# Kernel optimization log

Hardware: AMD Instinct MI355X
Metric: run time of the kernel (lower is better)

The kernel has to match this reference:

```python
import jax, jax.numpy as jnp
import numpy as np

N = 100000   # nodes
E = 1600000  # edges
DIN, DH, DOUT = 64, 128, 128


def setup_inputs() -> dict:
    key = jax.random.key(0)
    ks = jax.random.split(key, 12)
    x = jax.random.normal(ks[0], (N, DIN), dtype=jnp.float32)
    edge_index = jax.random.randint(ks[1], (2, E), 0, N, dtype=jnp.int32)
    s = 1.0 / np.sqrt(DIN)
    W1 = jax.random.uniform(ks[2], (DIN, DH), jnp.float32, -s, s)
    b1 = jnp.zeros((DH,), jnp.float32)
    g1 = jnp.ones((DH,), jnp.float32)
    bt1 = jnp.zeros((DH,), jnp.float32)
    s2 = 1.0 / np.sqrt(DH)
    W2 = jax.random.uniform(ks[3], (DH, DOUT), jnp.float32, -s2, s2)
    b2 = jnp.zeros((DOUT,), jnp.float32)
    g2 = jnp.ones((DOUT,), jnp.float32)
    bt2 = jnp.zeros((DOUT,), jnp.float32)
    return {"x": x, "edge_index": edge_index, "W1": W1, "b1": b1, "g1": g1,
            "bt1": bt1, "W2": W2, "b2": b2, "g2": g2, "bt2": bt2}


def _layer_norm(h, g, b, eps=1e-5):
    mu = h.mean(-1, keepdims=True)
    var = h.var(-1, keepdims=True)
    return (h - mu) * jax.lax.rsqrt(var + eps) * g + b


def reference(x, edge_index, W1, b1, g1, bt1, W2, b2, g2, bt2):
    # GCN normalization with self-loops (shared graph structure for both layers)
    src, dst = edge_index[0], edge_index[1]
    loops = jnp.arange(N, dtype=src.dtype)
    src = jnp.concatenate([src, loops])
    dst = jnp.concatenate([dst, loops])
    deg = jax.ops.segment_sum(jnp.ones_like(src, jnp.float32), dst, num_segments=N)
    dinv = jnp.where(deg > 0, jax.lax.rsqrt(deg), 0.0)
    norm = dinv[src] * dinv[dst]  # [E+N]

    def gcn(h, W, b):
        hw = h @ W                         # linear first (PyG GCNConv)
        msg = hw[src] * norm[:, None]      # gather + edge scale
        return jax.ops.segment_sum(msg, dst, num_segments=N) + b

    h = jax.nn.relu(_layer_norm(gcn(x, W1, b1), g1, bt1))
    # dropout is identity at inference
    h = jax.nn.relu(_layer_norm(gcn(h, W2, b2), g2, bt2))
    return h
```

## Files before the change

### kernel.cpp

```cpp
#include <hip/hip_runtime.h>

#define NN 100000
#define NE 1600000
#define NBKT 196
#define CAP 12288
#define EPB 2048
#define ABLK ((NE + EPB - 1) / EPB)
typedef unsigned short u16;
typedef unsigned int u32;

typedef __attribute__((ext_vector_type(8))) short short8v;
typedef __attribute__((ext_vector_type(4))) float f32x4;

__device__ __forceinline__ u32 f2bf(float f) {
    u32 u = __float_as_uint(f);
    return (u + 0x7fffu + ((u >> 16) & 1u)) >> 16;
}
__device__ __forceinline__ u32 pack2(float a, float b) {
    return f2bf(a) | (f2bf(b) << 16);
}
__device__ __forceinline__ void accum8(float* a, uint4 u, float w) {
    a[0] += __uint_as_float(u.x << 16) * w;
    a[1] += __uint_as_float(u.x & 0xffff0000u) * w;
    a[2] += __uint_as_float(u.y << 16) * w;
    a[3] += __uint_as_float(u.y & 0xffff0000u) * w;
    a[4] += __uint_as_float(u.z << 16) * w;
    a[5] += __uint_as_float(u.z & 0xffff0000u) * w;
    a[6] += __uint_as_float(u.w << 16) * w;
    a[7] += __uint_as_float(u.w & 0xffff0000u) * w;
}

__global__ __launch_bounds__(256) void kA_bin(const int* __restrict__ src,
                                              const int* __restrict__ dst,
                                              int* __restrict__ gcnt,
                                              u32* __restrict__ binned) {
    __shared__ int bc[NBKT];
    __shared__ int cbase[NBKT];
    const int tid = threadIdx.x;
    for (int i = tid; i < NBKT; i += 256) bc[i] = 0;
    __syncthreads();
    const int e0 = blockIdx.x * EPB;
#pragma unroll
    for (int i = 0; i < EPB / 256; ++i) {
        const int e = e0 + i * 256 + tid;
        if (e < NE) atomicAdd(&bc[dst[e] >> 9], 1);
    }
    __syncthreads();
    for (int i = tid; i < NBKT; i += 256)
        cbase[i] = bc[i] ? atomicAdd(&gcnt[i], bc[i]) : 0;
    __syncthreads();
    for (int i = tid; i < NBKT; i += 256) bc[i] = 0;
    __syncthreads();
#pragma unroll
    for (int i = 0; i < EPB / 256; ++i) {
        const int e = e0 + i * 256 + tid;
        if (e < NE) {
            const int d = dst[e];
            const int bkt = d >> 9;
            const int p = atomicAdd(&bc[bkt], 1);
            binned[bkt * CAP + cbase[bkt] + p] = ((u32)src[e] << 9) | (u32)(d & 511);
        }
    }
}

__global__ __launch_bounds__(256) void kB_fill(const u32* __restrict__ binned,
                                               const int* __restrict__ gcnt,
                                               int2* __restrict__ off2,
                                               float* __restrict__ dinv,
                                               int* __restrict__ csr,
                                               const float* __restrict__ x,
                                               u16* __restrict__ xb) {
    __shared__ int lcnt[512];
    __shared__ int lpos[512];
    __shared__ float sdinv[512];
    __shared__ int ws[4];
    const int b = blockIdx.x;
    const int tid = threadIdx.x;
    const int cnt = gcnt[b];
    const int base0 = b * CAP;
    const int node0 = b << 9;
    lcnt[tid] = 0;
    lcnt[tid + 256] = 0;
    __syncthreads();
    for (int e = tid; e < cnt; e += 256)
        atomicAdd(&lcnt[binned[base0 + e] & 511], 1);
    __syncthreads();
    const int c0 = lcnt[tid * 2], c1 = lcnt[tid * 2 + 1];
    const int s = c0 + c1;
    const int lane = tid & 63, w = tid >> 6;
    int incl = s;
#pragma unroll
    for (int o = 1; o < 64; o <<= 1) {
        const int u = __shfl_up(incl, o);
        if (lane >= o) incl += u;
    }
    if (lane == 63) ws[w] = incl;
    __syncthreads();
    int base = incl - s;
    for (int i = 0; i < w; ++i) base += ws[i];
    lpos[tid * 2] = base;
    lpos[tid * 2 + 1] = base + c0;
    const float d0 = rsqrtf(1.0f + (float)c0);
    const float d1 = rsqrtf(1.0f + (float)c1);
    sdinv[tid * 2] = d0;
    sdinv[tid * 2 + 1] = d1;
    const int n0 = node0 + tid * 2;
    if (n0 < NN) {
        off2[n0] = make_int2(base0 + base, base0 + base + c0);
        dinv[n0] = d0;
    }
    if (n0 + 1 < NN) {
        off2[n0 + 1] = make_int2(base0 + base + c0, base0 + base + c0 + c1);
        dinv[n0 + 1] = d1;
    }
    __syncthreads();
    for (int e = tid; e < cnt; e += 256) {
        const u32 u = binned[base0 + e];
        const int p = atomicAdd(&lpos[u & 511], 1);
        csr[base0 + p] = (int)(u >> 9);
    }
    const int nmax = min(512, NN - node0);
    for (int gi = tid; gi < nmax * 8; gi += 256) {
        const int nl = gi >> 3, ch = gi & 7;
        const float dr = sdinv[nl];
        const size_t xo = (size_t)(node0 + nl) * 64 + ch * 8;
        const float4 v0 = *(const float4*)&x[xo];
        const float4 v1 = *(const float4*)&x[xo + 4];
        uint4 o;
        o.x = pack2(v0.x * dr, v0.y * dr); o.y = pack2(v0.z * dr, v0.w * dr);
        o.z = pack2(v1.x * dr, v1.y * dr); o.w = pack2(v1.z * dr, v1.w * dr);
        *(uint4*)&xb[xo] = o;
    }
}

__global__ __launch_bounds__(256) void k_prep(const float* __restrict__ W1,
                                              const float* __restrict__ W2,
                                              u16* __restrict__ WT1,
                                              u16* __restrict__ WT2,
                                              int* __restrict__ gcnt) {
    const int i = blockIdx.x * 256 + threadIdx.x;
    if (i < 8192) {
        const int k = i >> 7, c = i & 127;
        WT1[c * 64 + k] = (u16)f2bf(W1[i]);
    } else if (i < 24576) {
        const int i2 = i - 8192;
        const int k = i2 >> 7, c = i2 & 127;
        WT2[c * 128 + k] = (u16)f2bf(W2[i2]);
    } else if (i < 24576 + NBKT) {
        gcnt[i - 24576] = 0;
    }
}

template<int K, bool FP32OUT, bool PRESCALE>
__global__ __launch_bounds__(256) void k_fused(const u16* __restrict__ A,
                                               const int2* __restrict__ off2,
                                               const int* __restrict__ csr,
                                               const float* __restrict__ dinv,
                                               const u16* __restrict__ WT,
                                               const float* __restrict__ bias,
                                               const float* __restrict__ g,
                                               const float* __restrict__ bt,
                                               void* __restrict__ outp) {
    constexpr int RB = K * 2;
    constexpr int SUBS = 512 / K;
    constexpr int LSH = (K == 64) ? 7 : 8;
    __shared__ u16 As[4 * 16 * K];
    const int tid = threadIdx.x;
    const int wv = tid >> 6, lane = tid & 63;
    const int sub = lane / (64 / SUBS);
    const int l = lane & (64 / SUBS - 1);
    const char* Ab = (const char*)A + ((u32)l << 4);
    char* myAs = (char*)As + wv * 16 * RB;
    const int nodeBase = blockIdx.x * 64 + wv * 16;

    for (int i = 0; i < 16; ++i) {
        const int node = min(nodeBase + i, NN - 1);
        const float di = dinv[node];
        float a[8] = {};
        {
            const uint4 u = *(const uint4*)(Ab + ((u32)node << LSH));
            accum8(a, u, (sub == 0) ? 1.0f : 0.0f);
        }
        const int2 oe = off2[node];
        int base = oe.x;
        const int e1 = oe.y;
        u32 iA = 0, iB = 0, iC = 0;
        float vA = 0.f, vB = 0.f, vC = 0.f;
        if (base < e1) {
            const int eA = base + sub, eB = eA + SUBS, eC = eA + 2 * SUBS;
            iA = (u32)csr[min(eA, e1 - 1)];
            iB = (u32)csr[min(eB, e1 - 1)];
            iC = (u32)csr[min(eC, e1 - 1)];
            vA = (eA < e1) ? 1.f : 0.f;
            vB = (eB < e1) ? 1.f : 0.f;
            vC = (eC < e1) ? 1.f : 0.f;
        }
        while (base < e1) {
            const uint4 uA = *(const uint4*)(Ab + (iA << LSH));
            const uint4 uB = *(const uint4*)(Ab + (iB << LSH));
            const uint4 uC = *(const uint4*)(Ab + (iC << LSH));
            const float wA = vA, wB = vB, wC = vC;
            base += 3 * SUBS;
            if (base < e1) {
                const int eA = base + sub, eB = eA + SUBS, eC = eA + 2 * SUBS;
                iA = (u32)csr[min(eA, e1 - 1)];
                iB = (u32)csr[min(eB, e1 - 1)];
                iC = (u32)csr[min(eC, e1 - 1)];
                vA = (eA < e1) ? 1.f : 0.f;
                vB = (eB < e1) ? 1.f : 0.f;
                vC = (eC < e1) ? 1.f : 0.f;
            }
            accum8(a, uA, wA);
            accum8(a, uB, wB);
            accum8(a, uC, wC);
        }
#pragma unroll
        for (int t = 0; t < 8; ++t)
#pragma unroll
            for (int o = 64 / SUBS; o < 64; o <<= 1)
                a[t] += __shfl_xor(a[t], o);
        if (sub == 0) {
            uint4 o;
            o.x = pack2(a[0] * di, a[1] * di); o.y = pack2(a[2] * di, a[3] * di);
            o.z = pack2(a[4] * di, a[5] * di); o.w = pack2(a[6] * di, a[7] * di);
            *(uint4*)(myAs + i * RB + (((u32)l << 4) ^ ((u32)(i & 7) << 4))) = o;
        }
    }

    const int lr = lane & 15, kg = lane >> 4;
    short8v af[K / 32];
#pragma unroll
    for (int kk = 0; kk < K / 32; ++kk)
        af[kk] = *(const short8v*)(myAs + lr * RB +
                                   ((u32)(kk * 64 + kg * 16) ^ ((u32)(lr & 7) << 4)));
    f32x4 acc[8];
#pragma unroll
    for (int nt = 0; nt < 8; ++nt) {
        acc[nt] = (f32x4){0.f, 0.f, 0.f, 0.f};
        const int col = nt * 16 + lr;
        short8v bf[K / 32];
#pragma unroll
        for (int kk = 0; kk < K / 32; ++kk)
            bf[kk] = *(const short8v*)&WT[col * K + kk * 32 + kg * 8];
#pragma unroll
        for (int kk = 0; kk < K / 32; ++kk)
            acc[nt] = __builtin_amdgcn_mfma_f32_16x16x32_bf16(af[kk], bf[kk], acc[nt], 0, 0, 0);
    }

    float s1[4] = {0.f, 0.f, 0.f, 0.f};
    float s2[4] = {0.f, 0.f, 0.f, 0.f};
#pragma unroll
    for (int nt = 0; nt < 8; ++nt) {
        const float bvn = bias[nt * 16 + lr];
#pragma unroll
        for (int j = 0; j < 4; ++j) {
            const float v = acc[nt][j] + bvn;
            acc[nt][j] = v;
            s1[j] += v;
            s2[j] += v * v;
        }
    }
#pragma unroll
    for (int j = 0; j < 4; ++j)
#pragma unroll
        for (int o = 1; o < 16; o <<= 1) {
            s1[j] += __shfl_xor(s1[j], o);
            s2[j] += __shfl_xor(s2[j], o);
        }
    float mu4[4], rs4[4], dr4[4];
    int wr4[4];
#pragma unroll
    for (int j = 0; j < 4; ++j) {
        const int node = nodeBase + kg * 4 + j;
        wr4[j] = node < NN;
        const float mu = s1[j] * (1.0f / 128.0f);
        const float var = s2[j] * (1.0f / 128.0f) - mu * mu;
        mu4[j] = mu;
        rs4[j] = rsqrtf(var + 1e-5f);
        dr4[j] = PRESCALE ? dinv[min(node, NN - 1)] : 1.0f;
    }
#pragma unroll
    for (int nt = 0; nt < 8; ++nt) {
        const int col = nt * 16 + lr;
        const float gvn = g[col];
        const float tvn = bt[col];
#pragma unroll
        for (int j = 0; j < 4; ++j) {
            if (wr4[j]) {
                const int node = nodeBase + kg * 4 + j;
                const float y = fmaxf((acc[nt][j] - mu4[j]) * rs4[j] * gvn + tvn, 0.f) * dr4[j];
                if constexpr (FP32OUT)
                    ((float*)outp)[(size_t)node * 128 + col] = y;
                else
                    ((u16*)outp)[(size_t)node * 128 + col] = (u16)f2bf(y);
            }
        }
    }
}

extern "C" void kernel_launch(void* const* d_in, const int* in_sizes, int n_in,
                              void* d_out, int out_size, void* d_ws, size_t ws_size,
                              hipStream_t stream) {
    const float* x   = (const float*)d_in[0];
    const int*   ei  = (const int*)d_in[1];
    const float* W1  = (const float*)d_in[2];
    const float* b1  = (const float*)d_in[3];
    const float* g1  = (const float*)d_in[4];
    const float* bt1 = (const float*)d_in[5];
    const float* W2  = (const float*)d_in[6];
    const float* b2  = (const float*)d_in[7];
    const float* g2  = (const float*)d_in[8];
    const float* bt2 = (const float*)d_in[9];

    const int* src = ei;
    const int* dst = ei + NE;

    const int NP = (NN + 255) & ~255;
    int*   gcnt   = (int*)d_ws;
    int2*  off2   = (int2*)(gcnt + 256);
    float* dinv   = (float*)(off2 + NP);
    int*   csr    = (int*)(dinv + NP);
    u32*   binned = (u32*)(csr + NBKT * CAP);
    u16*   xb     = (u16*)(binned + NBKT * CAP);
    u16*   h1     = xb + (size_t)NN * 64;
    u16*   WT1    = h1 + (size_t)NN * 128;
    u16*   WT2    = WT1 + 128 * 64;

    k_prep<<<(24576 + NBKT + 255) / 256, 256, 0, stream>>>(W1, W2, WT1, WT2, gcnt);
    kA_bin<<<ABLK, 256, 0, stream>>>(src, dst, gcnt, binned);
    kB_fill<<<NBKT, 256, 0, stream>>>(binned, gcnt, off2, dinv, csr, x, xb);

    k_fused<64, false, true><<<(NN + 63) / 64, 256, 0, stream>>>(
        xb, off2, csr, dinv, WT1, b1, g1, bt1, h1);

    k_fused<128, true, false><<<(NN + 63) / 64, 256, 0, stream>>>(
        h1, off2, csr, dinv, WT2, b2, g2, bt2, d_out);
}
```

Baseline: 236.5 us.

## Balance gather across waves via LDS work claiming and split GEMM columns

Each block now handles 32 nodes instead of 64. Waves claim nodes dynamically through an LDS atomic counter, so uneven per-node degrees no longer leave some waves idle while others finish their fixed 16-node slice. The MFMA stage is repartitioned so each wave computes 32 output columns for all 32 rows. Because of this the LayerNorm statistics are reduced across waves through shared memory, which adds two block barriers and an LDS reduction. The bounds clamps are dropped, which relies on NN being divisible by 32.

```diff
diff --git a/kernel.cpp b/kernel.cpp
--- a/kernel.cpp
+++ b/kernel.cpp
@@ -164,17 +164,25 @@
     constexpr int RB = K * 2;
     constexpr int SUBS = 512 / K;
     constexpr int LSH = (K == 64) ? 7 : 8;
-    __shared__ u16 As[4 * 16 * K];
+    __shared__ u16 As[32 * K];
+    __shared__ float s1s[4][32];
+    __shared__ float s2s[4][32];
+    __shared__ int claim;
     const int tid = threadIdx.x;
     const int wv = tid >> 6, lane = tid & 63;
     const int sub = lane / (64 / SUBS);
     const int l = lane & (64 / SUBS - 1);
     const char* Ab = (const char*)A + ((u32)l << 4);
-    char* myAs = (char*)As + wv * 16 * RB;
-    const int nodeBase = blockIdx.x * 64 + wv * 16;
-
-    for (int i = 0; i < 16; ++i) {
-        const int node = min(nodeBase + i, NN - 1);
+    const int nodeBase = blockIdx.x * 32;
+
+    if (tid == 0) claim = 0;
+    __syncthreads();
+
+    int i;
+    if (lane == 0) i = atomicAdd(&claim, 1);
+    i = __builtin_amdgcn_readfirstlane(i);
+    while (i < 32) {
+        const int node = nodeBase + i;
         const float di = dinv[node];
         float a[8] = {};
         {
@@ -223,79 +231,96 @@
             uint4 o;
             o.x = pack2(a[0] * di, a[1] * di); o.y = pack2(a[2] * di, a[3] * di);
             o.z = pack2(a[4] * di, a[5] * di); o.w = pack2(a[6] * di, a[7] * di);
-            *(uint4*)(myAs + i * RB + (((u32)l << 4) ^ ((u32)(i & 7) << 4))) = o;
-        }
-    }
+            *(uint4*)((char*)As + i * RB + (((u32)l << 4) ^ ((u32)(i & 7) << 4))) = o;
+        }
+        if (lane == 0) i = atomicAdd(&claim, 1);
+        i = __builtin_amdgcn_readfirstlane(i);
+    }
+    __syncthreads();
 
     const int lr = lane & 15, kg = lane >> 4;
-    short8v af[K / 32];
-#pragma unroll
-    for (int kk = 0; kk < K / 32; ++kk)
-        af[kk] = *(const short8v*)(myAs + lr * RB +
-                                   ((u32)(kk * 64 + kg * 16) ^ ((u32)(lr & 7) << 4)));
-    f32x4 acc[8];
-#pragma unroll
-    for (int nt = 0; nt < 8; ++nt) {
-        acc[nt] = (f32x4){0.f, 0.f, 0.f, 0.f};
-        const int col = nt * 16 + lr;
+    short8v af[2][K / 32];
+#pragma unroll
+    for (int rt = 0; rt < 2; ++rt)
+#pragma unroll
+        for (int kk = 0; kk < K / 32; ++kk)
+            af[rt][kk] = *(const short8v*)((const char*)As + (rt * 16 + lr) * RB +
+                                           ((u32)(kk * 64 + kg * 16) ^ ((u32)(lr & 7) << 4)));
+    f32x4 acc[2][2];
+    float bv[2], gv[2], tv[2];
+#pragma unroll
+    for (int nt = 0; nt < 2; ++nt) {
+        acc[0][nt] = (f32x4){0.f, 0.f, 0.f, 0.f};
+        acc[1][nt] = (f32x4){0.f, 0.f, 0.f, 0.f};
+        const int col = wv * 32 + nt * 16 + lr;
         short8v bf[K / 32];
 #pragma unroll
         for (int kk = 0; kk < K / 32; ++kk)
             bf[kk] = *(const short8v*)&WT[col * K + kk * 32 + kg * 8];
 #pragma unroll
-        for (int kk = 0; kk < K / 32; ++kk)
-            acc[nt] = __builtin_amdgcn_mfma_f32_16x16x32_bf16(af[kk], bf[kk], acc[nt], 0, 0, 0);
-    }
-
-    float s1[4] = {0.f, 0.f, 0.f, 0.f};
-    float s2[4] = {0.f, 0.f, 0.f, 0.f};
-#pragma unroll
-    for (int nt = 0; nt < 8; ++nt) {
-        const float bvn = bias[nt * 16 + lr];
+        for (int rt = 0; rt < 2; ++rt)
+#pragma unroll
+            for (int kk = 0; kk < K / 32; ++kk)
+                acc[rt][nt] = __builtin_amdgcn_mfma_f32_16x16x32_bf16(
+                    af[rt][kk], bf[kk], acc[rt][nt], 0, 0, 0);
+        bv[nt] = bias[col]; gv[nt] = g[col]; tv[nt] = bt[col];
+    }
+
+    float s1[2][4] = {};
+    float s2[2][4] = {};
+#pragma unroll
+    for (int rt = 0; rt < 2; ++rt)
+#pragma unroll
+        for (int nt = 0; nt < 2; ++nt)
+#pragma unroll
+            for (int j = 0; j < 4; ++j) {
+                const float v = acc[rt][nt][j] + bv[nt];
+                acc[rt][nt][j] = v;
+                s1[rt][j] += v;
+                s2[rt][j] += v * v;
+            }
+#pragma unroll
+    for (int rt = 0; rt < 2; ++rt)
+#pragma unroll
+        for (int j = 0; j < 4; ++j)
+#pragma unroll
+            for (int o = 1; o < 16; o <<= 1) {
+                s1[rt][j] += __shfl_xor(s1[rt][j], o);
+                s2[rt][j] += __shfl_xor(s2[rt][j], o);
+            }
+    if (lr == 0) {
+#pragma unroll
+        for (int rt = 0; rt < 2; ++rt)
+#pragma unroll
+            for (int j = 0; j < 4; ++j) {
+                s1s[wv][rt * 16 + kg * 4 + j] = s1[rt][j];
+                s2s[wv][rt * 16 + kg * 4 + j] = s2[rt][j];
+            }
+    }
+    __syncthreads();
+
+#pragma unroll
+    for (int rt = 0; rt < 2; ++rt)
 #pragma unroll
         for (int j = 0; j < 4; ++j) {
-            const float v = acc[nt][j] + bvn;
-            acc[nt][j] = v;
-            s1[j] += v;
-            s2[j] += v * v;
-        }
-    }
-#pragma unroll
-    for (int j = 0; j < 4; ++j)
-#pragma unroll
-        for (int o = 1; o < 16; o <<= 1) {
-            s1[j] += __shfl_xor(s1[j], o);
-            s2[j] += __shfl_xor(s2[j], o);
-        }
-    float mu4[4], rs4[4], dr4[4];
-    int wr4[4];
-#pragma unroll
-    for (int j = 0; j < 4; ++j) {
-        const int node = nodeBase + kg * 4 + j;
-        wr4[j] = node < NN;
-        const float mu = s1[j] * (1.0f / 128.0f);
-        const float var = s2[j] * (1.0f / 128.0f) - mu * mu;
-        mu4[j] = mu;
-        rs4[j] = rsqrtf(var + 1e-5f);
-        dr4[j] = PRESCALE ? dinv[min(node, NN - 1)] : 1.0f;
-    }
-#pragma unroll
-    for (int nt = 0; nt < 8; ++nt) {
-        const int col = nt * 16 + lr;
-        const float gvn = g[col];
-        const float tvn = bt[col];
-#pragma unroll
-        for (int j = 0; j < 4; ++j) {
-            if (wr4[j]) {
-                const int node = nodeBase + kg * 4 + j;
-                const float y = fmaxf((acc[nt][j] - mu4[j]) * rs4[j] * gvn + tvn, 0.f) * dr4[j];
+            const int row = rt * 16 + kg * 4 + j;
+            const float t1 = s1s[0][row] + s1s[1][row] + s1s[2][row] + s1s[3][row];
+            const float t2 = s2s[0][row] + s2s[1][row] + s2s[2][row] + s2s[3][row];
+            const float mu = t1 * (1.0f / 128.0f);
+            const float var = t2 * (1.0f / 128.0f) - mu * mu;
+            const float rs = rsqrtf(var + 1e-5f);
+            const int node = nodeBase + row;
+            const float dr = PRESCALE ? dinv[node] : 1.0f;
+#pragma unroll
+            for (int nt = 0; nt < 2; ++nt) {
+                const float y = fmaxf((acc[rt][nt][j] - mu) * rs * gv[nt] + tv[nt], 0.f) * dr;
+                const int col = wv * 32 + nt * 16 + lr;
                 if constexpr (FP32OUT)
                     ((float*)outp)[(size_t)node * 128 + col] = y;
                 else
                     ((u16*)outp)[(size_t)node * 128 + col] = (u16)f2bf(y);
             }
         }
-    }
 }
 
 extern "C" void kernel_launch(void* const* d_in, const int* in_sizes, int n_in,
@@ -330,9 +355,9 @@
     kA_bin<<<ABLK, 256, 0, stream>>>(src, dst, gcnt, binned);
     kB_fill<<<NBKT, 256, 0, stream>>>(binned, gcnt, off2, dinv, csr, x, xb);
 
-    k_fused<64, false, true><<<(NN + 63) / 64, 256, 0, stream>>>(
+    k_fused<64, false, true><<<NN / 32, 256, 0, stream>>>(
         xb, off2, csr, dinv, WT1, b1, g1, bt1, h1);
 
-    k_fused<128, true, false><<<(NN + 63) / 64, 256, 0, stream>>>(
+    k_fused<128, true, false><<<NN / 32, 256, 0, stream>>>(
         h1, off2, csr, dinv, WT2, b2, g2, bt2, d_out);
 }
```

Result: faster. 201.2 us (-15.0%).

## Dynamically distribute block's 64 nodes across wavefronts via LDS atomic counter

Applied to the files above, without the earlier changes.

Replaces the static assignment of 16 nodes per wavefront with a shared-memory atomic work counter, so each of the 4 wavefronts claims the next node to aggregate until all 64 are done. The goal is to balance uneven per-node degree across wavefronts within a block and reduce idle time before the MFMA stage. In exchange it adds an LDS atomic and readfirstlane per node plus a block-wide barrier before the matmul, since rows can now be written by any wavefront.

```diff
diff --git a/kernel.cpp b/kernel.cpp
--- a/kernel.cpp
+++ b/kernel.cpp
@@ -164,43 +164,35 @@
     constexpr int RB = K * 2;
     constexpr int SUBS = 512 / K;
     constexpr int LSH = (K == 64) ? 7 : 8;
-    __shared__ u16 As[4 * 16 * K];
+    __shared__ u16 As[64 * K];
+    __shared__ int claim;
     const int tid = threadIdx.x;
     const int wv = tid >> 6, lane = tid & 63;
     const int sub = lane / (64 / SUBS);
     const int l = lane & (64 / SUBS - 1);
     const char* Ab = (const char*)A + ((u32)l << 4);
-    char* myAs = (char*)As + wv * 16 * RB;
-    const int nodeBase = blockIdx.x * 64 + wv * 16;
-
-    for (int i = 0; i < 16; ++i) {
-        const int node = min(nodeBase + i, NN - 1);
-        const float di = dinv[node];
-        float a[8] = {};
-        {
-            const uint4 u = *(const uint4*)(Ab + ((u32)node << LSH));
-            accum8(a, u, (sub == 0) ? 1.0f : 0.0f);
-        }
-        const int2 oe = off2[node];
-        int base = oe.x;
-        const int e1 = oe.y;
-        u32 iA = 0, iB = 0, iC = 0;
-        float vA = 0.f, vB = 0.f, vC = 0.f;
-        if (base < e1) {
-            const int eA = base + sub, eB = eA + SUBS, eC = eA + 2 * SUBS;
-            iA = (u32)csr[min(eA, e1 - 1)];
-            iB = (u32)csr[min(eB, e1 - 1)];
-            iC = (u32)csr[min(eC, e1 - 1)];
-            vA = (eA < e1) ? 1.f : 0.f;
-            vB = (eB < e1) ? 1.f : 0.f;
-            vC = (eC < e1) ? 1.f : 0.f;
-        }
-        while (base < e1) {
-            const uint4 uA = *(const uint4*)(Ab + (iA << LSH));
-            const uint4 uB = *(const uint4*)(Ab + (iB << LSH));
-            const uint4 uC = *(const uint4*)(Ab + (iC << LSH));
-            const float wA = vA, wB = vB, wC = vC;
-            base += 3 * SUBS;
+    const int nodeBase = blockIdx.x * 64;
+
+    if (tid == 0) claim = 0;
+    __syncthreads();
+
+    int i;
+    if (lane == 0) i = atomicAdd(&claim, 1);
+    i = __builtin_amdgcn_readfirstlane(i);
+    while (i < 64) {
+        const int node = nodeBase + i;
+        if (node < NN) {
+            const float di = dinv[node];
+            float a[8] = {};
+            {
+                const uint4 u = *(const uint4*)(Ab + ((u32)node << LSH));
+                accum8(a, u, (sub == 0) ? 1.0f : 0.0f);
+            }
+            const int2 oe = off2[node];
+            int base = oe.x;
+            const int e1 = oe.y;
+            u32 iA = 0, iB = 0, iC = 0;
+            float vA = 0.f, vB = 0.f, vC = 0.f;
             if (base < e1) {
                 const int eA = base + sub, eB = eA + SUBS, eC = eA + 2 * SUBS;
                 iA = (u32)csr[min(eA, e1 - 1)];
@@ -210,29 +202,54 @@
                 vB = (eB < e1) ? 1.f : 0.f;
                 vC = (eC < e1) ? 1.f : 0.f;
             }
-            accum8(a, uA, wA);
-            accum8(a, uB, wB);
-            accum8(a, uC, wC);
-        }
-#pragma unroll
-        for (int t = 0; t < 8; ++t)
-#pragma unroll
-            for (int o = 64 / SUBS; o < 64; o <<= 1)
-                a[t] += __shfl_xor(a[t], o);
-        if (sub == 0) {
-            uint4 o;
-            o.x = pack2(a[0] * di, a[1] * di); o.y = pack2(a[2] * di, a[3] * di);
-            o.z = pack2(a[4] * di, a[5] * di); o.w = pack2(a[6] * di, a[7] * di);
-            *(uint4*)(myAs + i * RB + (((u32)l << 4) ^ ((u32)(i & 7) << 4))) = o;
-        }
-    }
+            while (base < e1) {
+                const uint4 uA = *(const uint4*)(Ab + (iA << LSH));
+                const uint4 uB = *(const uint4*)(Ab + (iB << LSH));
+                const uint4 uC = *(const uint4*)(Ab + (iC << LSH));
+                const float wA = vA, wB = vB, wC = vC;
+                base += 3 * SUBS;
+                if (base < e1) {
+                    const int eA = base + sub, eB = eA + SUBS, eC = eA + 2 * SUBS;
+                    iA = (u32)csr[min(eA, e1 - 1)];
+                    iB = (u32)csr[min(eB, e1 - 1)];
+                    iC = (u32)csr[min(eC, e1 - 1)];
+                    vA = (eA < e1) ? 1.f : 0.f;
+                    vB = (eB < e1) ? 1.f : 0.f;
+                    vC = (eC < e1) ? 1.f : 0.f;
+                }
+                accum8(a, uA, wA);
+                accum8(a, uB, wB);
+                accum8(a, uC, wC);
+            }
+#pragma unroll
+            for (int t = 0; t < 8; ++t)
+#pragma unroll
+                for (int o = 64 / SUBS; o < 64; o <<= 1)
+                    a[t] += __shfl_xor(a[t], o);
+            if (sub == 0) {
+                uint4 o;
+                o.x = pack2(a[0] * di, a[1] * di); o.y = pack2(a[2] * di, a[3] * di);
+                o.z = pack2(a[4] * di, a[5] * di); o.w = pack2(a[6] * di, a[7] * di);
+                *(uint4*)((char*)As + i * RB + (((u32)l << 4) ^ ((u32)(i & 7) << 4))) = o;
+            }
+        } else if (sub == 0) {
+            const uint4 z = make_uint4(0, 0, 0, 0);
+            *(uint4*)((char*)As + i * RB + (((u32)l << 4) ^ ((u32)(i & 7) << 4))) = z;
+        }
+        if (lane == 0) i = atomicAdd(&claim, 1);
+        i = __builtin_amdgcn_readfirstlane(i);
+    }
+    __syncthreads();
 
     const int lr = lane & 15, kg = lane >> 4;
+    const int rbase = wv * 16;
     short8v af[K / 32];
 #pragma unroll
-    for (int kk = 0; kk < K / 32; ++kk)
-        af[kk] = *(const short8v*)(myAs + lr * RB +
-                                   ((u32)(kk * 64 + kg * 16) ^ ((u32)(lr & 7) << 4)));
+    for (int kk = 0; kk < K / 32; ++kk) {
+        const int row = rbase + lr;
+        af[kk] = *(const short8v*)((const char*)As + row * RB +
+                                   ((u32)(kk * 64 + kg * 16) ^ ((u32)(row & 7) << 4)));
+    }
     f32x4 acc[8];
 #pragma unroll
     for (int nt = 0; nt < 8; ++nt) {
@@ -271,7 +288,7 @@
     int wr4[4];
 #pragma unroll
     for (int j = 0; j < 4; ++j) {
-        const int node = nodeBase + kg * 4 + j;
+        const int node = nodeBase + rbase + kg * 4 + j;
         wr4[j] = node < NN;
         const float mu = s1[j] * (1.0f / 128.0f);
         const float var = s2[j] * (1.0f / 128.0f) - mu * mu;
@@ -287,7 +304,7 @@
 #pragma unroll
         for (int j = 0; j < 4; ++j) {
             if (wr4[j]) {
-                const int node = nodeBase + kg * 4 + j;
+                const int node = nodeBase + rbase + kg * 4 + j;
                 const float y = fmaxf((acc[nt][j] - mu4[j]) * rs4[j] * gvn + tvn, 0.f) * dr4[j];
                 if constexpr (FP32OUT)
                     ((float*)outp)[(size_t)node * 128 + col] = y;
```

New measurement: 248.4 us. 1.05x slower.
